# Kernel tuning notes

Measured on AMD Instinct MI355X. Metric: run time of the kernel, lower is better.

The kernel has to match this reference:

```python
import jax, jax.numpy as jnp
import numpy as np

K = 128
HEADS = 8
B = 4
T = 2048


def setup_inputs() -> dict:
    key = jax.random.key(0)
    ks = jax.random.split(key, 6)
    x = jax.random.normal(ks[0], (B, T, K), dtype=jnp.float32)
    s = 1.0 / np.sqrt(K)
    # torch nn.Linear weights are (out_features, in_features)
    Wq = jax.random.uniform(ks[1], (HEADS * K, K), dtype=jnp.float32, minval=-s, maxval=s)
    Wk = jax.random.uniform(ks[2], (HEADS * K, K), dtype=jnp.float32, minval=-s, maxval=s)
    Wv = jax.random.uniform(ks[3], (HEADS * K, K), dtype=jnp.float32, minval=-s, maxval=s)
    su = 1.0 / np.sqrt(HEADS * K)
    Wu = jax.random.uniform(ks[4], (K, HEADS * K), dtype=jnp.float32, minval=-su, maxval=su)
    bu = jax.random.uniform(ks[5], (K,), dtype=jnp.float32, minval=-su, maxval=su)
    return {"x": x, "Wq": Wq, "Wk": Wk, "Wv": Wv, "Wu": Wu, "bu": bu}


def reference(x, Wq, Wk, Wv, Wu, bu):
    b, t, k = x.shape
    h = HEADS
    # project: Linear(k, k*h) then view(b,t,h,k); weight reshaped to (h, k_out, k_in)
    q = jnp.einsum('btk,hdk->bhtd', x, Wq.reshape(h, k, k))
    kk = jnp.einsum('btk,hdk->bhtd', x, Wk.reshape(h, k, k))
    v = jnp.einsum('btk,hdk->bhtd', x, Wv.reshape(h, k, k))
    scale = jnp.asarray(k, x.dtype) ** 0.25
    q = q / scale
    kk = kk / scale
    dot = jnp.einsum('bhtd,bhsd->bhts', q, kk)  # [b,h,t,t]
    att = jax.nn.softmax(dot, axis=-1)
    out = jnp.einsum('bhts,bhsd->bhtd', att, v)  # [b,h,t,k]
    out = out.transpose(0, 2, 1, 3).reshape(b, t, h * k)
    return out @ Wu.T + bu
```

## Files before the change

### kernel.cpp

```cpp
#include <hip/hip_runtime.h>
#include <cmath>

namespace {

constexpr int HEADS = 8;
constexpr int Bn = 4;
constexpr int Tn = 2048;
constexpr int Dn = 128;
constexpr float Q_PRESCALE = 0.1275174340f;

typedef _Float16 half8 __attribute__((ext_vector_type(8)));
typedef _Float16 half4 __attribute__((ext_vector_type(4)));
typedef float f32x4 __attribute__((ext_vector_type(4)));

__global__ __launch_bounds__(256) void cast_kernel(
    const float* __restrict__ x, const float* __restrict__ Wq, const float* __restrict__ Wk,
    const float* __restrict__ Wv, const float* __restrict__ Wu, _Float16* __restrict__ xh,
    _Float16* __restrict__ WH) {
  const int idx = blockIdx.x * 256 + threadIdx.x;
  const size_t base = (size_t)idx * 8;
  const float* src;
  _Float16* dst;
  if (base < 1048576) {
    src = x + base;
    dst = xh + base;
  } else {
    const size_t r = base - 1048576;
    const int s = (int)(r >> 17);
    src = ((s == 0) ? Wq : (s == 1) ? Wk : (s == 2) ? Wv : Wu) + (r & 131071);
    dst = WH + r;
  }
  const float4 a = *reinterpret_cast<const float4*>(src);
  const float4 b = *reinterpret_cast<const float4*>(src + 4);
  half8 h;
  h[0] = (_Float16)a.x; h[1] = (_Float16)a.y; h[2] = (_Float16)a.z; h[3] = (_Float16)a.w;
  h[4] = (_Float16)b.x; h[5] = (_Float16)b.y; h[6] = (_Float16)b.z; h[7] = (_Float16)b.w;
  *reinterpret_cast<half8*>(dst) = h;
}

__global__ __launch_bounds__(256, 4) void proj_kernel(const _Float16* __restrict__ xh,
                                                      const _Float16* __restrict__ WH,
                                                      _Float16* __restrict__ Qh,
                                                      _Float16* __restrict__ Kh,
                                                      _Float16* __restrict__ Vt) {
  __shared__ _Float16 sB[128 * 136];
  const int tid = threadIdx.x;
  const int w = tid >> 6, lane = tid & 63, quad = lane >> 4, l16 = lane & 15;
  const int m0 = blockIdx.x * 128;
  const int n0 = blockIdx.y * 128;

#pragma unroll
  for (int it = 0; it < 8; ++it) {
    const int fid = tid + it * 256;
    const int r = fid >> 4, g = fid & 15;
    const half8 v = *reinterpret_cast<const half8*>(WH + (size_t)(n0 + r) * 128 + g * 8);
    const int p = g ^ (r & 15);
    *reinterpret_cast<half8*>(sB + r * 128 + p * 8) = v;
  }

  half8 af[2][4];
  const _Float16* xp = xh + (size_t)(m0 + w * 32 + l16) * 128 + quad * 8;
#pragma unroll
  for (int mt = 0; mt < 2; ++mt)
#pragma unroll
    for (int kk = 0; kk < 4; ++kk)
      af[mt][kk] = *reinterpret_cast<const half8*>(xp + mt * 16 * 128 + kk * 32);

  __syncthreads();

  f32x4 acc[2][8];
#pragma unroll
  for (int mt = 0; mt < 2; ++mt)
#pragma unroll
    for (int nt = 0; nt < 8; ++nt) acc[mt][nt] = (f32x4){0.f, 0.f, 0.f, 0.f};

#pragma unroll
  for (int kk = 0; kk < 4; ++kk)
#pragma unroll
    for (int nt = 0; nt < 8; ++nt) {
      const int r = nt * 16 + l16;
      const int p = (kk * 4 + quad) ^ l16;
      const half8 bf = *reinterpret_cast<const half8*>(sB + r * 128 + p * 8);
      acc[0][nt] = __builtin_amdgcn_mfma_f32_16x16x32_f16(af[0][kk], bf, acc[0][nt], 0, 0, 0);
      acc[1][nt] = __builtin_amdgcn_mfma_f32_16x16x32_f16(af[1][kk], bf, acc[1][nt], 0, 0, 0);
    }

  const int sel = n0 >> 10;
  const int h = (n0 >> 7) & 7;
  const int b = m0 >> 11;
  const int t0b = m0 & 2047;
  const int bh = b * HEADS + h;
  const float scale = (sel == 0) ? Q_PRESCALE : 1.0f;

  __syncthreads();

  if (sel < 2) {
#pragma unroll
    for (int mt = 0; mt < 2; ++mt)
#pragma unroll
      for (int nt = 0; nt < 8; ++nt)
#pragma unroll
        for (int r = 0; r < 4; ++r)
          sB[(w * 32 + mt * 16 + quad * 4 + r) * 136 + nt * 16 + l16] =
              (_Float16)(acc[mt][nt][r] * scale);
  } else {
#pragma unroll
    for (int mt = 0; mt < 2; ++mt)
#pragma unroll
      for (int nt = 0; nt < 8; ++nt)
#pragma unroll
        for (int r = 0; r < 4; ++r)
          sB[(nt * 16 + l16) * 136 + w * 32 + mt * 16 + quad * 4 + r] = (_Float16)acc[mt][nt][r];
  }
  __syncthreads();

  _Float16* dstbase;
  size_t rstride;
  if (sel == 0) {
    dstbase = Qh + ((size_t)bh * Tn + t0b) * Dn;
    rstride = Dn;
  } else if (sel == 1) {
    dstbase = Kh + ((size_t)bh * Tn + t0b) * Dn;
    rstride = Dn;
  } else {
    dstbase = Vt + ((size_t)bh * Dn) * Tn + t0b;
    rstride = Tn;
  }
#pragma unroll
  for (int it = 0; it < 8; ++it) {
    const int fid = tid + it * 256;
    const int r = fid >> 4, g = fid & 15;
    const half8 v = *reinterpret_cast<const half8*>(sB + r * 136 + g * 8);
    *reinterpret_cast<half8*>(dstbase + (size_t)r * rstride + g * 8) = v;
  }
}

__global__ __launch_bounds__(256, 2) void flash_kernel(const _Float16* __restrict__ Qh,
                                                       const _Float16* __restrict__ Kh,
                                                       const _Float16* __restrict__ Vt,
                                                       _Float16* __restrict__ Obh) {
  __shared__ _Float16 sK[64 * 128];
  __shared__ _Float16 sV[128 * 64];
  __shared__ _Float16 sP[4][32 * 64];
  __shared__ float sL[4][2][16];

  const int tid = threadIdx.x;
  const int w = tid >> 6;
  const int lane = tid & 63;
  const int quad = lane >> 4;
  const int l16 = lane & 15;
  const int qt = blockIdx.x;
  const int bh = blockIdx.y;

  half8 qf[2][4];
#pragma unroll
  for (int qg = 0; qg < 2; ++qg) {
    const _Float16* Qp =
        Qh + ((size_t)bh * Tn + qt * 128 + w * 32 + qg * 16 + l16) * Dn + quad * 8;
#pragma unroll
    for (int kk = 0; kk < 4; ++kk) qf[qg][kk] = *reinterpret_cast<const half8*>(Qp + kk * 32);
  }

  const _Float16* Kp = Kh + (size_t)bh * Tn * Dn;
  const _Float16* Vp = Vt + (size_t)bh * Dn * Tn;
  _Float16* sPw = sP[w];

  f32x4 o[2][8];
#pragma unroll
  for (int qg = 0; qg < 2; ++qg)
#pragma unroll
    for (int nt = 0; nt < 8; ++nt) o[qg][nt] = (f32x4){0.f, 0.f, 0.f, 0.f};
  float lsum[2] = {0.f, 0.f};

  half8 kreg[4], vreg[4];
  const int kr = tid >> 4, kg = tid & 15;
  const int vr = tid >> 3, vg = tid & 7;
#pragma unroll
  for (int it = 0; it < 4; ++it) {
    kreg[it] = *reinterpret_cast<const half8*>(Kp + (size_t)(kr + it * 16) * Dn + kg * 8);
    vreg[it] = *reinterpret_cast<const half8*>(Vp + (size_t)(vr + it * 32) * Tn + vg * 8);
  }

  for (int st = 0; st < Tn / 64; ++st) {
    __syncthreads();
#pragma unroll
    for (int it = 0; it < 4; ++it) {
      const int r = kr + it * 16;
      const int p = kg ^ (r & 15);
      *reinterpret_cast<half8*>(sK + r * 128 + p * 8) = kreg[it];
      const int rv = vr + it * 32;
      const int pv = vg ^ ((rv & 7) ^ ((rv >> 1) & 4));
      *reinterpret_cast<half8*>(sV + rv * 64 + pv * 8) = vreg[it];
    }
    if (st + 1 < Tn / 64) {
      const _Float16* knext = Kp + (size_t)(st + 1) * 64 * Dn;
      const _Float16* vnext = Vp + (st + 1) * 64;
#pragma unroll
      for (int it = 0; it < 4; ++it) {
        kreg[it] = *reinterpret_cast<const half8*>(knext + (size_t)(kr + it * 16) * Dn + kg * 8);
        vreg[it] = *reinterpret_cast<const half8*>(vnext + (size_t)(vr + it * 32) * Tn + vg * 8);
      }
    }
    __syncthreads();

    f32x4 s_t[2][4];
#pragma unroll
    for (int qg = 0; qg < 2; ++qg)
#pragma unroll
      for (int j = 0; j < 4; ++j) s_t[qg][j] = (f32x4){0.f, 0.f, 0.f, 0.f};
#pragma unroll
    for (int kk = 0; kk < 4; ++kk)
#pragma unroll
      for (int j = 0; j < 4; ++j) {
        const int p = (kk * 4 + quad) ^ l16;
        const half8 kf = *reinterpret_cast<const half8*>(sK + (j * 16 + l16) * 128 + p * 8);
        s_t[0][j] = __builtin_amdgcn_mfma_f32_16x16x32_f16(kf, qf[0][kk], s_t[0][j], 0, 0, 0);
        s_t[1][j] = __builtin_amdgcn_mfma_f32_16x16x32_f16(kf, qf[1][kk], s_t[1][j], 0, 0, 0);
      }

#pragma unroll
    for (int qg = 0; qg < 2; ++qg)
#pragma unroll
      for (int j = 0; j < 4; ++j) {
        f32x4 e;
        e[0] = __builtin_amdgcn_exp2f(s_t[qg][j][0]);
        e[1] = __builtin_amdgcn_exp2f(s_t[qg][j][1]);
        e[2] = __builtin_amdgcn_exp2f(s_t[qg][j][2]);
        e[3] = __builtin_amdgcn_exp2f(s_t[qg][j][3]);
        lsum[qg] += (e[0] + e[1]) + (e[2] + e[3]);
        half4 h4;
        h4[0] = (_Float16)e[0]; h4[1] = (_Float16)e[1];
        h4[2] = (_Float16)e[2]; h4[3] = (_Float16)e[3];
        const int g = j * 2 + (quad >> 1);
        const int p = g ^ (l16 & 7);
        *reinterpret_cast<half4*>(sPw + (qg * 16 + l16) * 64 + p * 8 + (quad & 1) * 4) = h4;
      }

#pragma unroll
    for (int kk2 = 0; kk2 < 2; ++kk2) {
      half8 pf[2];
#pragma unroll
      for (int qg = 0; qg < 2; ++qg) {
        const int pA = (kk2 * 4 + quad) ^ (l16 & 7);
        pf[qg] = *reinterpret_cast<const half8*>(sPw + (qg * 16 + l16) * 64 + pA * 8);
      }
#pragma unroll
      for (int nt = 0; nt < 8; ++nt) {
        const int r = nt * 16 + l16;
        const int pV = (kk2 * 4 + quad) ^ ((r & 7) ^ ((r >> 1) & 4));
        const half8 vf = *reinterpret_cast<const half8*>(sV + r * 64 + pV * 8);
        o[0][nt] = __builtin_amdgcn_mfma_f32_16x16x32_f16(pf[0], vf, o[0][nt], 0, 0, 0);
        o[1][nt] = __builtin_amdgcn_mfma_f32_16x16x32_f16(pf[1], vf, o[1][nt], 0, 0, 0);
      }
    }
  }

#pragma unroll
  for (int qg = 0; qg < 2; ++qg) {
    float ls = lsum[qg];
    ls += __shfl_xor(ls, 16);
    ls += __shfl_xor(ls, 32);
    if (quad == 0) sL[w][qg][l16] = 1.0f / ls;
  }
  const int b = bh >> 3, h = bh & 7;
#pragma unroll
  for (int qg = 0; qg < 2; ++qg) {
    const f32x4 inv4 = *reinterpret_cast<const f32x4*>(&sL[w][qg][quad * 4]);
#pragma unroll
    for (int r = 0; r < 4; ++r) {
      const size_t trow =
          (size_t)(b * Tn + qt * 128 + w * 32 + qg * 16 + quad * 4 + r) * (HEADS * Dn);
#pragma unroll
      for (int nt = 0; nt < 8; ++nt)
        Obh[trow + h * Dn + nt * 16 + l16] = (_Float16)(o[qg][nt][r] * inv4[r]);
    }
  }
}

__global__ __launch_bounds__(256, 4) void outproj_kernel(const _Float16* __restrict__ Obh,
                                                         const _Float16* __restrict__ Wuh,
                                                         const float* __restrict__ bu,
                                                         float* __restrict__ out) {
  __shared__ float sR[4 * 32 * 128];
  const int tid = threadIdx.x;
  const int w = tid >> 6, lane = tid & 63, quad = lane >> 4, l16 = lane & 15;
  const int r0 = blockIdx.x * 32;

  f32x4 acc[2][8];
#pragma unroll
  for (int mt = 0; mt < 2; ++mt)
#pragma unroll
    for (int nt = 0; nt < 8; ++nt) acc[mt][nt] = (f32x4){0.f, 0.f, 0.f, 0.f};

  const _Float16* ap = Obh + (size_t)(r0 + l16) * 1024 + w * 256 + quad * 8;
  const _Float16* bp = Wuh + (size_t)l16 * 1024 + w * 256 + quad * 8;

#pragma unroll
  for (int kk = 0; kk < 8; ++kk) {
    const half8 a0 = *reinterpret_cast<const half8*>(ap + kk * 32);
    const half8 a1 = *reinterpret_cast<const half8*>(ap + 16 * 1024 + kk * 32);
#pragma unroll
    for (int nt = 0; nt < 8; ++nt) {
      const half8 bf = *reinterpret_cast<const half8*>(bp + (size_t)nt * 16 * 1024 + kk * 32);
      acc[0][nt] = __builtin_amdgcn_mfma_f32_16x16x32_f16(a0, bf, acc[0][nt], 0, 0, 0);
      acc[1][nt] = __builtin_amdgcn_mfma_f32_16x16x32_f16(a1, bf, acc[1][nt], 0, 0, 0);
    }
  }

#pragma unroll
  for (int mt = 0; mt < 2; ++mt)
#pragma unroll
    for (int nt = 0; nt < 8; ++nt)
#pragma unroll
      for (int r = 0; r < 4; ++r)
        sR[w * 4096 + (mt * 16 + quad * 4 + r) * 128 + nt * 16 + l16] = acc[mt][nt][r];
  __syncthreads();

#pragma unroll
  for (int it = 0; it < 16; ++it) {
    const int idx = tid + it * 256;
    const int row = idx >> 7, col = idx & 127;
    const float v = sR[idx] + sR[4096 + idx] + sR[8192 + idx] + sR[12288 + idx] + bu[col];
    out[(size_t)(r0 + row) * Dn + col] = v;
  }
}

}

extern "C" void kernel_launch(void* const* d_in, const int* in_sizes, int n_in, void* d_out,
                              int out_size, void* d_ws, size_t ws_size, hipStream_t stream) {
  (void)in_sizes; (void)n_in; (void)out_size; (void)ws_size;
  const float* x = (const float*)d_in[0];
  const float* Wq = (const float*)d_in[1];
  const float* Wk = (const float*)d_in[2];
  const float* Wv = (const float*)d_in[3];
  const float* Wu = (const float*)d_in[4];
  const float* bu = (const float*)d_in[5];
  float* out = (float*)d_out;

  constexpr size_t NE = (size_t)Bn * HEADS * Tn * Dn;
  char* ws = (char*)d_ws;
  _Float16* xh = (_Float16*)ws;
  _Float16* WH = (_Float16*)(ws + 2097152);
  _Float16* Qh = (_Float16*)(ws + 4194304);
  _Float16* Kh = (_Float16*)(ws + 4194304 + NE * 2);
  _Float16* Vt = (_Float16*)(ws + 4194304 + NE * 4);
  _Float16* Obh = (_Float16*)(ws + 4194304 + NE * 6);
  _Float16* Wuh = WH + 393216;

  cast_kernel<<<dim3(768), 256, 0, stream>>>(x, Wq, Wk, Wv, Wu, xh, WH);
  proj_kernel<<<dim3(64, 24), 256, 0, stream>>>(xh, WH, Qh, Kh, Vt);
  flash_kernel<<<dim3(16, 32), 256, 0, stream>>>(Qh, Kh, Vt, Obh);
  outproj_kernel<<<dim3(256), 256, 0, stream>>>(Obh, Wuh, bu, out);
}
```

Measured before the change: 176.3 us.

## Split flash attention over two KV halves and merge partials in out-projection

The flash kernel now splits the key/value sequence into two halves along a new grid dimension. Each half writes unnormalized partial outputs (scaled by a fixed constant) and row sums, so the grid doubles from 512 to 1024 blocks and occupancy is raised to 3 blocks per CU. The out-projection kernel sums the two partials, normalizes them by the combined row sums and then runs the GEMM, with a smaller 16-row tile per block. This relies on the softmax using a fixed max (no running max), and it costs extra global traffic for the second partial buffer.

```diff
diff --git a/kernel.cpp b/kernel.cpp
--- a/kernel.cpp
+++ b/kernel.cpp
@@ -8,6 +8,8 @@
 constexpr int Tn = 2048;
 constexpr int Dn = 128;
 constexpr float Q_PRESCALE = 0.1275174340f;
+constexpr float OSCALE = 0.015625f;
+constexpr size_t NE = (size_t)Bn * HEADS * Tn * Dn;
 
 typedef _Float16 half8 __attribute__((ext_vector_type(8)));
 typedef _Float16 half4 __attribute__((ext_vector_type(4)));
@@ -135,14 +137,14 @@
   }
 }
 
-__global__ __launch_bounds__(256, 2) void flash_kernel(const _Float16* __restrict__ Qh,
+__global__ __launch_bounds__(256, 3) void flash_kernel(const _Float16* __restrict__ Qh,
                                                        const _Float16* __restrict__ Kh,
                                                        const _Float16* __restrict__ Vt,
-                                                       _Float16* __restrict__ Obh) {
+                                                       _Float16* __restrict__ Opart,
+                                                       float* __restrict__ Lpart) {
   __shared__ _Float16 sK[64 * 128];
   __shared__ _Float16 sV[128 * 64];
   __shared__ _Float16 sP[4][32 * 64];
-  __shared__ float sL[4][2][16];
 
   const int tid = threadIdx.x;
   const int w = tid >> 6;
@@ -151,6 +153,8 @@
   const int l16 = lane & 15;
   const int qt = blockIdx.x;
   const int bh = blockIdx.y;
+  const int z = blockIdx.z;
+  const int st0 = z * 16, st1 = z * 16 + 16;
 
   half8 qf[2][4];
 #pragma unroll
@@ -177,11 +181,11 @@
   const int vr = tid >> 3, vg = tid & 7;
 #pragma unroll
   for (int it = 0; it < 4; ++it) {
-    kreg[it] = *reinterpret_cast<const half8*>(Kp + (size_t)(kr + it * 16) * Dn + kg * 8);
-    vreg[it] = *reinterpret_cast<const half8*>(Vp + (size_t)(vr + it * 32) * Tn + vg * 8);
-  }
-
-  for (int st = 0; st < Tn / 64; ++st) {
+    kreg[it] = *reinterpret_cast<const half8*>(Kp + (size_t)(st0 * 64 + kr + it * 16) * Dn + kg * 8);
+    vreg[it] = *reinterpret_cast<const half8*>(Vp + (size_t)(vr + it * 32) * Tn + st0 * 64 + vg * 8);
+  }
+
+  for (int st = st0; st < st1; ++st) {
     __syncthreads();
 #pragma unroll
     for (int it = 0; it < 4; ++it) {
@@ -192,7 +196,7 @@
       const int pv = vg ^ ((rv & 7) ^ ((rv >> 1) & 4));
       *reinterpret_cast<half8*>(sV + rv * 64 + pv * 8) = vreg[it];
     }
-    if (st + 1 < Tn / 64) {
+    if (st + 1 < st1) {
       const _Float16* knext = Kp + (size_t)(st + 1) * 64 * Dn;
       const _Float16* vnext = Vp + (st + 1) * 64;
 #pragma unroll
@@ -255,72 +259,78 @@
     }
   }
 
+  const int b = bh >> 3, h = bh & 7;
+  _Float16* Oz = Opart + (size_t)z * NE;
 #pragma unroll
   for (int qg = 0; qg < 2; ++qg) {
     float ls = lsum[qg];
     ls += __shfl_xor(ls, 16);
     ls += __shfl_xor(ls, 32);
-    if (quad == 0) sL[w][qg][l16] = 1.0f / ls;
-  }
-  const int b = bh >> 3, h = bh & 7;
-#pragma unroll
-  for (int qg = 0; qg < 2; ++qg) {
-    const f32x4 inv4 = *reinterpret_cast<const f32x4*>(&sL[w][qg][quad * 4]);
+    const int t = qt * 128 + w * 32 + qg * 16 + l16;
+    if (quad == 0) Lpart[(size_t)z * 65536 + ((size_t)b * Tn + t) * 8 + h] = ls;
 #pragma unroll
     for (int r = 0; r < 4; ++r) {
       const size_t trow =
           (size_t)(b * Tn + qt * 128 + w * 32 + qg * 16 + quad * 4 + r) * (HEADS * Dn);
 #pragma unroll
       for (int nt = 0; nt < 8; ++nt)
-        Obh[trow + h * Dn + nt * 16 + l16] = (_Float16)(o[qg][nt][r] * inv4[r]);
-    }
-  }
-}
-
-__global__ __launch_bounds__(256, 4) void outproj_kernel(const _Float16* __restrict__ Obh,
+        Oz[trow + h * Dn + nt * 16 + l16] = (_Float16)(o[qg][nt][r] * OSCALE);
+    }
+  }
+}
+
+__global__ __launch_bounds__(256, 4) void outproj_kernel(const _Float16* __restrict__ Opart,
+                                                         const float* __restrict__ Lpart,
                                                          const _Float16* __restrict__ Wuh,
                                                          const float* __restrict__ bu,
                                                          float* __restrict__ out) {
-  __shared__ float sR[4 * 32 * 128];
+  __shared__ float sR[4 * 16 * 128];
   const int tid = threadIdx.x;
   const int w = tid >> 6, lane = tid & 63, quad = lane >> 4, l16 = lane & 15;
-  const int r0 = blockIdx.x * 32;
-
-  f32x4 acc[2][8];
-#pragma unroll
-  for (int mt = 0; mt < 2; ++mt)
-#pragma unroll
-    for (int nt = 0; nt < 8; ++nt) acc[mt][nt] = (f32x4){0.f, 0.f, 0.f, 0.f};
-
-  const _Float16* ap = Obh + (size_t)(r0 + l16) * 1024 + w * 256 + quad * 8;
+  const int r0 = blockIdx.x * 16;
+  const int t = r0 + l16;
+
+  const int h0 = w * 2;
+  const float la = Lpart[(size_t)t * 8 + h0] + Lpart[65536 + (size_t)t * 8 + h0];
+  const float lb = Lpart[(size_t)t * 8 + h0 + 1] + Lpart[65536 + (size_t)t * 8 + h0 + 1];
+  const float inv0 = 64.0f / la;
+  const float inv1 = 64.0f / lb;
+
+  f32x4 acc[8];
+#pragma unroll
+  for (int nt = 0; nt < 8; ++nt) acc[nt] = (f32x4){0.f, 0.f, 0.f, 0.f};
+
+  const _Float16* a1p = Opart + (size_t)t * 1024 + w * 256 + quad * 8;
+  const _Float16* a2p = a1p + NE;
   const _Float16* bp = Wuh + (size_t)l16 * 1024 + w * 256 + quad * 8;
 
 #pragma unroll
   for (int kk = 0; kk < 8; ++kk) {
-    const half8 a0 = *reinterpret_cast<const half8*>(ap + kk * 32);
-    const half8 a1 = *reinterpret_cast<const half8*>(ap + 16 * 1024 + kk * 32);
+    const half8 x1 = *reinterpret_cast<const half8*>(a1p + kk * 32);
+    const half8 x2 = *reinterpret_cast<const half8*>(a2p + kk * 32);
+    const float sc = (kk < 4) ? inv0 : inv1;
+    half8 a0;
+#pragma unroll
+    for (int j = 0; j < 8; ++j) a0[j] = (_Float16)(((float)x1[j] + (float)x2[j]) * sc);
 #pragma unroll
     for (int nt = 0; nt < 8; ++nt) {
       const half8 bf = *reinterpret_cast<const half8*>(bp + (size_t)nt * 16 * 1024 + kk * 32);
-      acc[0][nt] = __builtin_amdgcn_mfma_f32_16x16x32_f16(a0, bf, acc[0][nt], 0, 0, 0);
-      acc[1][nt] = __builtin_amdgcn_mfma_f32_16x16x32_f16(a1, bf, acc[1][nt], 0, 0, 0);
-    }
-  }
-
-#pragma unroll
-  for (int mt = 0; mt < 2; ++mt)
-#pragma unroll
-    for (int nt = 0; nt < 8; ++nt)
-#pragma unroll
-      for (int r = 0; r < 4; ++r)
-        sR[w * 4096 + (mt * 16 + quad * 4 + r) * 128 + nt * 16 + l16] = acc[mt][nt][r];
+      acc[nt] = __builtin_amdgcn_mfma_f32_16x16x32_f16(a0, bf, acc[nt], 0, 0, 0);
+    }
+  }
+
+#pragma unroll
+  for (int nt = 0; nt < 8; ++nt)
+#pragma unroll
+    for (int r = 0; r < 4; ++r)
+      sR[w * 2048 + (quad * 4 + r) * 128 + nt * 16 + l16] = acc[nt][r];
   __syncthreads();
 
 #pragma unroll
-  for (int it = 0; it < 16; ++it) {
+  for (int it = 0; it < 8; ++it) {
     const int idx = tid + it * 256;
     const int row = idx >> 7, col = idx & 127;
-    const float v = sR[idx] + sR[4096 + idx] + sR[8192 + idx] + sR[12288 + idx] + bu[col];
+    const float v = sR[idx] + sR[2048 + idx] + sR[4096 + idx] + sR[6144 + idx] + bu[col];
     out[(size_t)(r0 + row) * Dn + col] = v;
   }
 }
@@ -338,18 +348,18 @@
   const float* bu = (const float*)d_in[5];
   float* out = (float*)d_out;
 
-  constexpr size_t NE = (size_t)Bn * HEADS * Tn * Dn;
   char* ws = (char*)d_ws;
   _Float16* xh = (_Float16*)ws;
   _Float16* WH = (_Float16*)(ws + 2097152);
   _Float16* Qh = (_Float16*)(ws + 4194304);
   _Float16* Kh = (_Float16*)(ws + 4194304 + NE * 2);
   _Float16* Vt = (_Float16*)(ws + 4194304 + NE * 4);
-  _Float16* Obh = (_Float16*)(ws + 4194304 + NE * 6);
+  _Float16* Opart = (_Float16*)(ws + 4194304 + NE * 6);
+  float* Lpart = (float*)(ws + 4194304 + NE * 10);
   _Float16* Wuh = WH + 393216;
 
   cast_kernel<<<dim3(768), 256, 0, stream>>>(x, Wq, Wk, Wv, Wu, xh, WH);
   proj_kernel<<<dim3(64, 24), 256, 0, stream>>>(xh, WH, Qh, Kh, Vt);
-  flash_kernel<<<dim3(16, 32), 256, 0, stream>>>(Qh, Kh, Vt, Obh);
-  outproj_kernel<<<dim3(256), 256, 0, stream>>>(Obh, Wuh, bu, out);
-}
+  flash_kernel<<<dim3(16, 32, 2), 256, 0, stream>>>(Qh, Kh, Vt, Opart, Lpart);
+  outproj_kernel<<<dim3(512), 256, 0, stream>>>(Opart, Lpart, Wuh, bu, out);
+}
```

New measurement: 299.9 us. +70.1%, slower.
